# Kernel optimization log

Measured on AMD Instinct MI355X. Metric: run time of the kernel, lower is better.

Reference implementation:

```python
import jax, jax.numpy as jnp
import numpy as np

B, S, H = 8, 2048, 512
M = 4096
TEMP = 0.1
EPS = 1e-6


def setup_inputs() -> dict:
    key = jax.random.key(0)
    ks = jax.random.split(key, 8)
    scale = 1.0 / np.sqrt(H)
    return {
        "hidden_states": jax.random.normal(ks[0], (B, S, H), dtype=jnp.float32),
        "memory_keys": jax.random.normal(ks[1], (M, H), dtype=jnp.float32),
        "memory_values": jax.random.normal(ks[2], (M, H), dtype=jnp.float32),
        "Wk": jax.random.normal(ks[3], (H, H), dtype=jnp.float32) * scale,
        "bk": jnp.zeros((H,), dtype=jnp.float32),
        "Wo": jax.random.normal(ks[4], (H, H), dtype=jnp.float32) * scale,
        "bo": jnp.zeros((H,), dtype=jnp.float32),
        "memory_usage": jax.random.randint(ks[5], (M,), 0, 2, dtype=jnp.int32),
    }


def reference(hidden_states, memory_keys, memory_values, Wk, bk, Wo, bo, memory_usage):
    # key projection: [B,S,H]
    q = jnp.einsum("bsh,kh->bsk", hidden_states, Wk) + bk
    # L2-style normalization with eps inside rsqrt (matches torch.rsqrt(norm_sq + 1e-6))
    q_n = q * jax.lax.rsqrt(jnp.sum(q * q, axis=-1, keepdims=True) + EPS)
    mk_n = memory_keys * jax.lax.rsqrt(
        jnp.sum(memory_keys * memory_keys, axis=-1, keepdims=True) + EPS
    )
    # cosine-similarity scores over the memory bank: [B,S,M]
    scores = jnp.einsum("bsk,mk->bsm", q_n, mk_n) / TEMP
    mask = (memory_usage > 0).astype(scores.dtype)  # [M]
    scores = scores * mask + (-1e9) * (1.0 - mask)
    attn = jax.nn.softmax(scores, axis=-1)  # [B,S,M]
    retrieved = jnp.einsum("bsm,mv->bsv", attn, memory_values)  # [B,S,H]
    out = jnp.einsum("bsv,hv->bsh", retrieved, Wo) + bo
    return out
```

## Files before the change

### kernel.cpp

```cpp
#include <hip/hip_runtime.h>
#include <cstdint>
#include <cstddef>

#define H_DIM   512
#define M_DIM   4096

typedef unsigned short u16;
typedef short bf16x8 __attribute__((ext_vector_type(8)));
typedef float f32x4  __attribute__((ext_vector_type(4)));

__device__ __forceinline__ u16 f2b(float f) {
  union { float f; uint32_t u; } v; v.f = f;
  uint32_t u = v.u + (0x7FFFu + ((v.u >> 16) & 1u));
  return (u16)(u >> 16);
}

__global__ void k_f2bf(const float* __restrict__ in, u16* __restrict__ out, int n4) {
  int i = blockIdx.x * blockDim.x + threadIdx.x;
  if (i < n4) {
    float4 v = ((const float4*)in)[i];
    ushort4 o;
    o.x = f2b(v.x); o.y = f2b(v.y); o.z = f2b(v.z); o.w = f2b(v.w);
    ((ushort4*)out)[i] = o;
  }
}

__global__ void k_f2bf_ww(const float* __restrict__ wk, const float* __restrict__ wo,
                          u16* __restrict__ owk, u16* __restrict__ owo) {
  int i = blockIdx.x * blockDim.x + threadIdx.x;
  const float* src = (i < 65536) ? wk : wo;
  u16* dst = (i < 65536) ? owk : owo;
  int j = i & 65535;
  float4 v = ((const float4*)src)[j];
  ushort4 o;
  o.x = f2b(v.x); o.y = f2b(v.y); o.z = f2b(v.z); o.w = f2b(v.w);
  ((ushort4*)dst)[j] = o;
}

__global__ void k_compact(const int* __restrict__ usage, int* __restrict__ idx,
                          int* __restrict__ meta) {
  __shared__ int cnt[256];
  int t = threadIdx.x;
  int base = t * 16;
  int c = 0;
  #pragma unroll
  for (int i = 0; i < 16; ++i) c += (usage[base + i] > 0) ? 1 : 0;
  cnt[t] = c;
  __syncthreads();
  for (int d = 1; d < 256; d <<= 1) {
    int v = (t >= d) ? cnt[t - d] : 0;
    __syncthreads();
    cnt[t] += v;
    __syncthreads();
  }
  int pos = cnt[t] - c;
  for (int i = 0; i < 16; ++i)
    if (usage[base + i] > 0) idx[pos++] = base + i;
  if (t == 0) {
    int total = cnt[255];
    int keff = ((total + 127) >> 7) << 7;
    meta[0] = total; meta[1] = keff; meta[2] = keff >> 5; meta[3] = keff >> 7;
  }
}

__global__ void k_gather_both(const float* __restrict__ keys, const float* __restrict__ vals,
                              const int* __restrict__ idx, const int* __restrict__ meta,
                              u16* __restrict__ okeys, u16* __restrict__ ovals) {
  int j    = blockIdx.x * 4 + (threadIdx.x >> 6);
  int lane = threadIdx.x & 63;
  int count = meta[0];
  ushort4* kp = (ushort4*)(okeys + (size_t)j * H_DIM);
  ushort4* vp = (ushort4*)(ovals + (size_t)j * H_DIM);
  if (j >= count) {
    ushort4 z = {0, 0, 0, 0};
    kp[lane] = z; kp[lane + 64] = z;
    vp[lane] = z; vp[lane + 64] = z;
    return;
  }
  int src = idx[j];
  const float4* rp = (const float4*)(keys + (size_t)src * H_DIM);
  float4 a = rp[lane];
  float4 b = rp[lane + 64];
  float ss = a.x*a.x + a.y*a.y + a.z*a.z + a.w*a.w
           + b.x*b.x + b.y*b.y + b.z*b.z + b.w*b.w;
  #pragma unroll
  for (int d = 1; d < 64; d <<= 1) ss += __shfl_xor(ss, d, 64);
  float s = rsqrtf(ss + 1e-6f);
  ushort4 oa, ob;
  oa.x = f2b(a.x*s); oa.y = f2b(a.y*s); oa.z = f2b(a.z*s); oa.w = f2b(a.w*s);
  ob.x = f2b(b.x*s); ob.y = f2b(b.y*s); ob.z = f2b(b.z*s); ob.w = f2b(b.w*s);
  kp[lane]      = oa;
  kp[lane + 64] = ob;
  const float4* vr = (const float4*)(vals + (size_t)src * H_DIM);
  float4 c0 = vr[lane];
  float4 c1 = vr[lane + 64];
  ushort4 va, vb;
  va.x = f2b(c0.x); va.y = f2b(c0.y); va.z = f2b(c0.z); va.w = f2b(c0.w);
  vb.x = f2b(c1.x); vb.y = f2b(c1.y); vb.z = f2b(c1.z); vb.w = f2b(c1.w);
  vp[lane]      = va;
  vp[lane + 64] = vb;
}

__global__ void k_rsq(const float* __restrict__ qss, float* __restrict__ rsq) {
  int r = blockIdx.x * blockDim.x + threadIdx.x;
  float s = 0.0f;
  #pragma unroll
  for (int i = 0; i < 8; ++i) s += qss[(size_t)r * 8 + i];
  rsq[r] = rsqrtf(s + 1e-6f);
}

__global__ void k_reduce_l(const float* __restrict__ lpart, float* __restrict__ linv,
                           const int* __restrict__ meta) {
  int r = blockIdx.x * blockDim.x + threadIdx.x;
  int n = meta[1] >> 6;
  float s = 0.0f;
  for (int i = 0; i < n; ++i) s += lpart[(size_t)r * 64 + i];
  linv[r] = 1.0f / s;
}

#define EPI_MW    1

template<int EPI>
__global__ __launch_bounds__(256, 3)
void k_gemm_bt(const u16* __restrict__ A, const u16* __restrict__ B,
               int N, int K,
               const int* __restrict__ meta,
               u16* __restrict__ outh) {
  __shared__ u16 Ah[2][128 * 32];
  __shared__ u16 Bh[2][128 * 32];

  const int tid  = threadIdx.x;
  const int wave = tid >> 6, lane = tid & 63;
  const int wr = (wave >> 1) * 64;
  const int wc = (wave & 1) * 64;

  int t0 = blockIdx.x, t_end = meta[1] >> 7, t_step = 16;
  int fixedb = blockIdx.y;
  const int kiters = K >> 5;

  const int srow   = lane & 15;
  const int schunk = lane >> 4;
  const int lds_off = schunk * 128 + srow * 8;

  const int fr = lane & 15;
  const int fbase = (lane >> 4) * 128 + fr * 8;
  const int g = lane >> 4;

  const char* Ac = (const char*)A;
  const char* Bc = (const char*)B;

  for (int t = t0; t < t_end; t += t_step) {
    const int row0 = fixedb << 7;
    const int col0 = t << 7;
    __syncthreads();

    uint32_t aB[2], bB[2];
    #pragma unroll
    for (int s2 = 0; s2 < 2; ++s2) {
      aB[s2] = (uint32_t)(((size_t)(row0 + (wave + s2 * 4) * 16 + srow) * (size_t)K
                           + (size_t)(schunk * 8)) * 2u);
      bB[s2] = (uint32_t)(((size_t)(col0 + (wave + s2 * 4) * 16 + srow) * (size_t)K
                           + (size_t)(schunk * 8)) * 2u);
    }

    f32x4 acc[4][4];
    const f32x4 z = {0.0f, 0.0f, 0.0f, 0.0f};
    #pragma unroll
    for (int i = 0; i < 4; ++i)
      #pragma unroll
      for (int j = 0; j < 4; ++j) acc[i][j] = z;

    bf16x8 rA[2], rB[2];
    auto gload = [&](int k0) {
      const uint32_t kb = (uint32_t)(k0 << 1);
      #pragma unroll
      for (int s2 = 0; s2 < 2; ++s2) rA[s2] = *(const bf16x8*)(Ac + aB[s2] + kb);
      #pragma unroll
      for (int s2 = 0; s2 < 2; ++s2) rB[s2] = *(const bf16x8*)(Bc + bB[s2] + kb);
    };

    gload(0);
    for (int it = 0; it < kiters; ++it) {
      const int cur = it & 1;
      #pragma unroll
      for (int s2 = 0; s2 < 2; ++s2)
        *(bf16x8*)&Ah[cur][(wave + s2 * 4) * 512 + lds_off] = rA[s2];
      #pragma unroll
      for (int s2 = 0; s2 < 2; ++s2)
        *(bf16x8*)&Bh[cur][(wave + s2 * 4) * 512 + lds_off] = rB[s2];
      if (it + 1 < kiters) gload((it + 1) << 5);
      __syncthreads();

      bf16x8 af[4], bfv[4];
      #pragma unroll
      for (int i = 0; i < 4; ++i)
        af[i] = *(const bf16x8*)&Ah[cur][((wr >> 4) + i) * 512 + fbase];
      #pragma unroll
      for (int j = 0; j < 4; ++j)
        bfv[j] = *(const bf16x8*)&Bh[cur][((wc >> 4) + j) * 512 + fbase];
      #pragma unroll
      for (int i = 0; i < 4; ++i)
        #pragma unroll
        for (int j = 0; j < 4; ++j)
          acc[i][j] = __builtin_amdgcn_mfma_f32_16x16x32_bf16(af[i], bfv[j], acc[i][j], 0, 0, 0);
    }

    #pragma unroll
    for (int i = 0; i < 4; ++i) {
      #pragma unroll
      for (int r = 0; r < 4; ++r) {
        int grow = row0 + wr + i * 16 + g * 4 + r;
        #pragma unroll
        for (int j = 0; j < 4; ++j) {
          int gcol = col0 + wc + j * 16 + fr;
          outh[(size_t)grow * (size_t)N + gcol] = f2b(acc[i][j][r]);
        }
      }
    }
  }
}

#define EPI2_P     0
#define EPI2_OUT   1
#define EPI2_QPROJ 2

template<int EPI>
__global__ __launch_bounds__(512, 2)
void k_gemm2(const u16* __restrict__ A, const u16* __restrict__ B,
             const int* __restrict__ meta,
             float* __restrict__ outf, u16* __restrict__ outh,
             const float* __restrict__ bias,
             float* __restrict__ aux,
             const float* __restrict__ rowscale) {
  constexpr int BM   = (EPI == EPI2_P) ? 256 : 128;
  constexpr int MF   = BM / 32;
  constexpr int NF   = 4;
  constexpr int APS  = BM / 128;
  constexpr int NLA  = BM / 64;
  constexpr int NLB  = 4;
  constexpr int ASUB = BM * 32;
  constexpr int BSUB = 256 * 32;

  __shared__ u16 Ah[2][BM * 64];
  __shared__ u16 Bh[2][256 * 64];

  const int tid  = threadIdx.x;
  const int wave = tid >> 6, lane = tid & 63;
  const int wave_m = wave >> 2, wave_n = wave & 3;
  const int wm0 = wave_m * (BM >> 1);
  const int wn0 = wave_n * 64;
  const int fr  = lane & 15, g = lane >> 4;
  const int fbase = g * 128 + fr * 8;

  int m0, r0, kel;
  if (EPI == EPI2_P) {
    int id = blockIdx.x + (blockIdx.y << 4);
    int xcd = id & 7, s = id >> 3;
    r0 = (xcd * 8 + (s >> 4)) << 8;
    m0 = (s & 15) << 8;
    if (m0 >= meta[1]) return;
    kel = 512;
  } else if (EPI == EPI2_OUT) {
    int id = blockIdx.x + (blockIdx.y << 2);
    int xcd = id & 7, s = id >> 3;
    r0 = (xcd * 8 + (s >> 2)) << 8;
    m0 = (s & 3) << 7;
    kel = meta[1];
  } else {
    int id = blockIdx.x + (blockIdx.y << 2);
    int xcd = id & 7, s = id >> 3;
    r0 = (xcd * 8 + (s >> 2)) << 8;
    m0 = (s & 3) << 7;
    kel = 512;
  }
  const int kiters = kel >> 6;
  if (kiters <= 0) return;
  const int kstr = (EPI == EPI2_OUT) ? M_DIM : 512;

  const char* Ac = (const char*)A;
  const char* Bc = (const char*)B;
  uint32_t aB[NLA], bB[NLB];
  #pragma unroll
  for (int s2 = 0; s2 < NLA; ++s2) {
    int ks = s2 / APS;
    int u  = tid + (s2 % APS) * 512;
    int row = ((u >> 6) << 4) + (u & 15);
    int kch = (u >> 4) & 3;
    aB[s2] = (uint32_t)(((size_t)(m0 + row) * (size_t)kstr
                         + (size_t)(ks * 32 + kch * 8)) * 2u);
  }
  #pragma unroll
  for (int s2 = 0; s2 < NLB; ++s2) {
    int ks = s2 >> 1;
    int u  = tid + (s2 & 1) * 512;
    int row = ((u >> 6) << 4) + (u & 15);
    int kch = (u >> 4) & 3;
    bB[s2] = (uint32_t)(((size_t)(r0 + row) * (size_t)kstr
                         + (size_t)(ks * 32 + kch * 8)) * 2u);
  }

  f32x4 acc[MF][NF];
  const f32x4 z = {0.0f, 0.0f, 0.0f, 0.0f};
  #pragma unroll
  for (int i = 0; i < MF; ++i)
    #pragma unroll
    for (int j = 0; j < NF; ++j) acc[i][j] = z;

  auto gload = [&](bf16x8 (&ra)[NLA], bf16x8 (&rb)[NLB], int it1) {
    const uint32_t kb = (uint32_t)(it1 << 7);
    #pragma unroll
    for (int s2 = 0; s2 < NLA; ++s2) ra[s2] = *(const bf16x8*)(Ac + aB[s2] + kb);
    #pragma unroll
    for (int s2 = 0; s2 < NLB; ++s2) rb[s2] = *(const bf16x8*)(Bc + bB[s2] + kb);
  };
  auto commit = [&](int cur, bf16x8 (&ra)[NLA], bf16x8 (&rb)[NLB]) {
    #pragma unroll
    for (int s2 = 0; s2 < NLA; ++s2)
      *(bf16x8*)&Ah[cur][(s2 / APS) * ASUB + (tid + (s2 % APS) * 512) * 8] = ra[s2];
    #pragma unroll
    for (int s2 = 0; s2 < NLB; ++s2)
      *(bf16x8*)&Bh[cur][(s2 >> 1) * BSUB + (tid + (s2 & 1) * 512) * 8] = rb[s2];
  };
  auto compute = [&](int cur) {
    bf16x8 af[MF], bfv[NF];
    #pragma unroll
    for (int i = 0; i < MF; ++i)
      af[i] = *(const bf16x8*)&Ah[cur][((wm0 >> 4) + i) * 512 + fbase];
    #pragma unroll
    for (int j = 0; j < NF; ++j)
      bfv[j] = *(const bf16x8*)&Bh[cur][((wn0 >> 4) + j) * 512 + fbase];
    #pragma unroll
    for (int i = 0; i < MF; ++i)
      #pragma unroll
      for (int j = 0; j < NF; ++j)
        acc[i][j] = __builtin_amdgcn_mfma_f32_16x16x32_bf16(af[i], bfv[j], acc[i][j], 0, 0, 0);
    #pragma unroll
    for (int i = 0; i < MF; ++i)
      af[i] = *(const bf16x8*)&Ah[cur][ASUB + ((wm0 >> 4) + i) * 512 + fbase];
    #pragma unroll
    for (int j = 0; j < NF; ++j)
      bfv[j] = *(const bf16x8*)&Bh[cur][BSUB + ((wn0 >> 4) + j) * 512 + fbase];
    #pragma unroll
    for (int i = 0; i < MF; ++i)
      #pragma unroll
      for (int j = 0; j < NF; ++j)
        acc[i][j] = __builtin_amdgcn_mfma_f32_16x16x32_bf16(af[i], bfv[j], acc[i][j], 0, 0, 0);
  };

  if constexpr (EPI == EPI2_P) {
    bf16x8 rA[NLA], rB[NLB];
    gload(rA, rB, 0);
    for (int it = 0; it < kiters; ++it) {
      const int cur = it & 1;
      commit(cur, rA, rB);
      if (it + 1 < kiters) gload(rA, rB, it + 1);
      __syncthreads();
      compute(cur);
    }
  } else {
    bf16x8 a0[NLA], b0[NLB], a1[NLA], b1[NLB];
    gload(a0, b0, 0);
    if (kiters > 1) gload(a1, b1, 1);
    for (int it = 0; it < kiters; it += 2) {
      commit(0, a0, b0);
      if (it + 2 < kiters) gload(a0, b0, it + 2);
      __syncthreads();
      compute(0);
      commit(1, a1, b1);
      if (it + 3 < kiters) gload(a1, b1, it + 3);
      __syncthreads();
      compute(1);
    }
  }

  if (EPI == EPI2_P) {
    const int count = meta[0];
    float rq10[NF];
    #pragma unroll
    for (int j = 0; j < NF; ++j)
      rq10[j] = rowscale[r0 + wn0 + j * 16 + fr] * 10.0f;
    float sj[NF] = {0.f, 0.f, 0.f, 0.f};
    #pragma unroll
    for (int i = 0; i < MF; ++i) {
      const int mb = m0 + wm0 + i * 16 + g * 4;
      #pragma unroll
      for (int j = 0; j < NF; ++j) {
        const size_t rr = (size_t)(r0 + wn0 + j * 16 + fr);
        float p0 = (mb + 0 < count) ? __expf(acc[i][j][0] * rq10[j]) : 0.0f;
        float p1 = (mb + 1 < count) ? __expf(acc[i][j][1] * rq10[j]) : 0.0f;
        float p2 = (mb + 2 < count) ? __expf(acc[i][j][2] * rq10[j]) : 0.0f;
        float p3 = (mb + 3 < count) ? __expf(acc[i][j][3] * rq10[j]) : 0.0f;
        ushort4 st; st.x = f2b(p0); st.y = f2b(p1); st.z = f2b(p2); st.w = f2b(p3);
        *(ushort4*)(outh + rr * M_DIM + mb) = st;
        sj[j] += (p0 + p1) + (p2 + p3);
      }
    }
    const int slot = (m0 + wm0) >> 6;
    #pragma unroll
    for (int j = 0; j < NF; ++j) {
      float s = sj[j];
      s += __shfl_xor(s, 16, 64);
      s += __shfl_xor(s, 32, 64);
      if (lane < 16) {
        const size_t rr = (size_t)(r0 + wn0 + j * 16 + lane);
        aux[rr * 64 + slot]     = s;
        aux[rr * 64 + slot + 1] = 0.0f;
      }
    }
  } else if (EPI == EPI2_OUT) {
    float scl[NF];
    #pragma unroll
    for (int j = 0; j < NF; ++j)
      scl[j] = rowscale[r0 + wn0 + j * 16 + fr];
    #pragma unroll
    for (int i = 0; i < MF; ++i) {
      const int hb = m0 + wm0 + i * 16 + g * 4;
      const float4 bv = *(const float4*)(bias + hb);
      #pragma unroll
      for (int j = 0; j < NF; ++j) {
        const size_t rr = (size_t)(r0 + wn0 + j * 16 + fr);
        float4 o;
        o.x = acc[i][j][0] * scl[j] + bv.x;
        o.y = acc[i][j][1] * scl[j] + bv.y;
        o.z = acc[i][j][2] * scl[j] + bv.z;
        o.w = acc[i][j][3] * scl[j] + bv.w;
        *(float4*)(outf + rr * H_DIM + hb) = o;
      }
    }
  } else {
    float sj[NF] = {0.f, 0.f, 0.f, 0.f};
    #pragma unroll
    for (int i = 0; i < MF; ++i) {
      const int kb = m0 + wm0 + i * 16 + g * 4;
      const float4 bkv = *(const float4*)(bias + kb);
      #pragma unroll
      for (int j = 0; j < NF; ++j) {
        const size_t rr = (size_t)(r0 + wn0 + j * 16 + fr);
        float v0 = acc[i][j][0] + bkv.x;
        float v1 = acc[i][j][1] + bkv.y;
        float v2 = acc[i][j][2] + bkv.z;
        float v3 = acc[i][j][3] + bkv.w;
        ushort4 st; st.x = f2b(v0); st.y = f2b(v1); st.z = f2b(v2); st.w = f2b(v3);
        *(ushort4*)(outh + rr * H_DIM + kb) = st;
        sj[j] += v0 * v0 + v1 * v1 + v2 * v2 + v3 * v3;
      }
    }
    const int slot = (m0 + wm0) >> 6;
    #pragma unroll
    for (int j = 0; j < NF; ++j) {
      float s = sj[j];
      s += __shfl_xor(s, 16, 64);
      s += __shfl_xor(s, 32, 64);
      if (lane < 16)
        aux[(size_t)(r0 + wn0 + j * 16 + lane) * 8 + slot] = s;
    }
  }
}

extern "C" void kernel_launch(void* const* d_in, const int* in_sizes, int n_in,
                              void* d_out, int out_size, void* d_ws, size_t ws_size,
                              hipStream_t stream) {
  const float* hidden = (const float*)d_in[0];
  const float* mkeys  = (const float*)d_in[1];
  const float* mvals  = (const float*)d_in[2];
  const float* Wk     = (const float*)d_in[3];
  const float* bk     = (const float*)d_in[4];
  const float* Wo     = (const float*)d_in[5];
  const float* bo     = (const float*)d_in[6];
  const int*   usage  = (const int*)d_in[7];
  (void)in_sizes; (void)n_in; (void)out_size; (void)ws_size;

  char* ws = (char*)d_ws;
  u16*   hb    = (u16*)(ws + 0);
  int*   idx   = (int*)(ws + 0);
  int*   meta  = (int*)(ws + 16384);
  float* lpart = (float*)(ws + 1048576);
  u16*   wkb   = (u16*)(ws + 16777216);
  u16*   wob   = (u16*)(ws + 17301504);
  u16*   mkn   = (u16*)(ws + 17825792);
  u16*   mv_c  = (u16*)(ws + 22020096);
  u16*   qb    = (u16*)(ws + 26214400);
  u16*   MWt   = (u16*)(ws + 42991616);
  u16*   P     = (u16*)(ws + 47185920);
  float* qss   = (float*)(ws + 47185920);
  float* rsqQ  = (float*)(ws + 181665792);
  float* linv  = (float*)(ws + 183828480);

  k_f2bf<<<8192, 256, 0, stream>>>(hidden, hb, 2097152);
  k_f2bf_ww<<<512, 256, 0, stream>>>(Wk, Wo, wkb, wob);

  k_gemm2<EPI2_QPROJ><<<dim3(4, 64), 512, 0, stream>>>(wkb, hb, nullptr,
      nullptr, qb, bk, qss, nullptr);
  k_rsq<<<64, 256, 0, stream>>>(qss, rsqQ);

  k_compact<<<1, 256, 0, stream>>>(usage, idx, meta);
  k_gather_both<<<1024, 256, 0, stream>>>(mkeys, mvals, idx, meta, mkn, mv_c);

  k_gemm_bt<EPI_MW><<<dim3(16, 4), 256, 0, stream>>>(wob, mv_c, M_DIM, 512,
      meta, MWt);

  k_gemm2<EPI2_P><<<dim3(16, 64), 512, 0, stream>>>(mkn, qb, meta,
      nullptr, P, nullptr, lpart, rsqQ);
  k_reduce_l<<<64, 256, 0, stream>>>(lpart, linv, meta);

  k_gemm2<EPI2_OUT><<<dim3(4, 64), 512, 0, stream>>>(MWt, P, meta,
      (float*)d_out, nullptr, bo, nullptr, linv);
}
```

Baseline: 256.0 us.

## Restructure GEMM main loop to overlap LDS commits with MFMA and raise priority

Reorders the double-buffered GEMM pipeline so the next tile's LDS commit and global prefetch happen between the two MFMA half-steps of the current tile, with one barrier per iteration instead of commit-then-sync-then-compute. It also wraps each MFMA block in s_setprio(1)/s_setprio(0) so matrix instructions get issue priority over other waves' memory work. The intent is to hide LDS write and global load latency behind MFMA execution. In exchange, fragment registers stay live longer across the loop, which raises register pressure, and the buffer hand-off needs correct ordering to avoid races.

```diff
diff --git a/kernel.cpp b/kernel.cpp
--- a/kernel.cpp
+++ b/kernel.cpp
@@ -306,6 +306,8 @@
     #pragma unroll
     for (int j = 0; j < NF; ++j) acc[i][j] = z;
 
+  bf16x8 af[MF], bfv[NF];
+
   auto gload = [&](bf16x8 (&ra)[NLA], bf16x8 (&rb)[NLB], int it1) {
     const uint32_t kb = (uint32_t)(it1 << 7);
     #pragma unroll
@@ -321,55 +323,61 @@
     for (int s2 = 0; s2 < NLB; ++s2)
       *(bf16x8*)&Bh[cur][(s2 >> 1) * BSUB + (tid + (s2 & 1) * 512) * 8] = rb[s2];
   };
-  auto compute = [&](int cur) {
-    bf16x8 af[MF], bfv[NF];
+  auto read_frags = [&](int cur, int ks) {
     #pragma unroll
     for (int i = 0; i < MF; ++i)
-      af[i] = *(const bf16x8*)&Ah[cur][((wm0 >> 4) + i) * 512 + fbase];
+      af[i] = *(const bf16x8*)&Ah[cur][ks * ASUB + ((wm0 >> 4) + i) * 512 + fbase];
     #pragma unroll
     for (int j = 0; j < NF; ++j)
-      bfv[j] = *(const bf16x8*)&Bh[cur][((wn0 >> 4) + j) * 512 + fbase];
+      bfv[j] = *(const bf16x8*)&Bh[cur][ks * BSUB + ((wn0 >> 4) + j) * 512 + fbase];
+  };
+  auto mfma_all = [&]() {
+    __builtin_amdgcn_s_setprio(1);
     #pragma unroll
     for (int i = 0; i < MF; ++i)
       #pragma unroll
       for (int j = 0; j < NF; ++j)
         acc[i][j] = __builtin_amdgcn_mfma_f32_16x16x32_bf16(af[i], bfv[j], acc[i][j], 0, 0, 0);
-    #pragma unroll
-    for (int i = 0; i < MF; ++i)
-      af[i] = *(const bf16x8*)&Ah[cur][ASUB + ((wm0 >> 4) + i) * 512 + fbase];
-    #pragma unroll
-    for (int j = 0; j < NF; ++j)
-      bfv[j] = *(const bf16x8*)&Bh[cur][BSUB + ((wn0 >> 4) + j) * 512 + fbase];
-    #pragma unroll
-    for (int i = 0; i < MF; ++i)
-      #pragma unroll
-      for (int j = 0; j < NF; ++j)
-        acc[i][j] = __builtin_amdgcn_mfma_f32_16x16x32_bf16(af[i], bfv[j], acc[i][j], 0, 0, 0);
+    __builtin_amdgcn_s_setprio(0);
   };
 
   if constexpr (EPI == EPI2_P) {
     bf16x8 rA[NLA], rB[NLB];
     gload(rA, rB, 0);
+    commit(0, rA, rB);
+    if (kiters > 1) gload(rA, rB, 1);
+    __syncthreads();
     for (int it = 0; it < kiters; ++it) {
       const int cur = it & 1;
-      commit(cur, rA, rB);
-      if (it + 1 < kiters) gload(rA, rB, it + 1);
+      read_frags(cur, 0);
+      mfma_all();
+      read_frags(cur, 1);
+      if (it + 1 < kiters) commit(cur ^ 1, rA, rB);
+      if (it + 2 < kiters) gload(rA, rB, it + 2);
+      mfma_all();
       __syncthreads();
-      compute(cur);
     }
   } else {
     bf16x8 a0[NLA], b0[NLB], a1[NLA], b1[NLB];
     gload(a0, b0, 0);
+    commit(0, a0, b0);
     if (kiters > 1) gload(a1, b1, 1);
+    __syncthreads();
     for (int it = 0; it < kiters; it += 2) {
-      commit(0, a0, b0);
+      read_frags(0, 0);
       if (it + 2 < kiters) gload(a0, b0, it + 2);
+      mfma_all();
+      read_frags(0, 1);
+      if (it + 1 < kiters) commit(1, a1, b1);
+      mfma_all();
       __syncthreads();
-      compute(0);
-      commit(1, a1, b1);
+      read_frags(1, 0);
       if (it + 3 < kiters) gload(a1, b1, it + 3);
+      mfma_all();
+      read_frags(1, 1);
+      if (it + 2 < kiters) commit(0, a0, b0);
+      mfma_all();
       __syncthreads();
-      compute(1);
     }
   }
 
```

Result: slower. 271.4 us (+6.0%).

## Fuse fp32-to-bf16 conversions and gathers into GEMM loads, drop rsq kernel

Applied to the files above, without the earlier changes.

The q-projection GEMM now reads fp32 hidden states directly and converts to bf16 while staging into LDS, which removes the separate conversion kernel and its bf16 intermediate. The memory-values gather and conversion are folded into the MW GEMM through indexed fp32 loads. The row-norm rsqrt reduction moves into the P-GEMM epilogue, so the small k_rsq kernel goes away. The fused loaders move twice the bytes per element through registers and the MW B-operand loads are now indirect, which could cut the efficiency of the inner loops.

```diff
diff --git a/kernel.cpp b/kernel.cpp
--- a/kernel.cpp
+++ b/kernel.cpp
@@ -15,14 +15,11 @@
   return (u16)(u >> 16);
 }
 
-__global__ void k_f2bf(const float* __restrict__ in, u16* __restrict__ out, int n4) {
-  int i = blockIdx.x * blockDim.x + threadIdx.x;
-  if (i < n4) {
-    float4 v = ((const float4*)in)[i];
-    ushort4 o;
-    o.x = f2b(v.x); o.y = f2b(v.y); o.z = f2b(v.z); o.w = f2b(v.w);
-    ((ushort4*)out)[i] = o;
-  }
+__device__ __forceinline__ bf16x8 cvt8(const float4& lo, const float4& hi) {
+  union { u16 u[8]; bf16x8 v; } o;
+  o.u[0] = f2b(lo.x); o.u[1] = f2b(lo.y); o.u[2] = f2b(lo.z); o.u[3] = f2b(lo.w);
+  o.u[4] = f2b(hi.x); o.u[5] = f2b(hi.y); o.u[6] = f2b(hi.z); o.u[7] = f2b(hi.w);
+  return o.v;
 }
 
 __global__ void k_f2bf_ww(const float* __restrict__ wk, const float* __restrict__ wo,
@@ -63,18 +60,16 @@
   }
 }
 
-__global__ void k_gather_both(const float* __restrict__ keys, const float* __restrict__ vals,
+__global__ void k_gather_keys(const float* __restrict__ keys,
                               const int* __restrict__ idx, const int* __restrict__ meta,
-                              u16* __restrict__ okeys, u16* __restrict__ ovals) {
+                              u16* __restrict__ okeys) {
   int j    = blockIdx.x * 4 + (threadIdx.x >> 6);
   int lane = threadIdx.x & 63;
   int count = meta[0];
   ushort4* kp = (ushort4*)(okeys + (size_t)j * H_DIM);
-  ushort4* vp = (ushort4*)(ovals + (size_t)j * H_DIM);
   if (j >= count) {
     ushort4 z = {0, 0, 0, 0};
     kp[lane] = z; kp[lane + 64] = z;
-    vp[lane] = z; vp[lane + 64] = z;
     return;
   }
   int src = idx[j];
@@ -91,22 +86,6 @@
   ob.x = f2b(b.x*s); ob.y = f2b(b.y*s); ob.z = f2b(b.z*s); ob.w = f2b(b.w*s);
   kp[lane]      = oa;
   kp[lane + 64] = ob;
-  const float4* vr = (const float4*)(vals + (size_t)src * H_DIM);
-  float4 c0 = vr[lane];
-  float4 c1 = vr[lane + 64];
-  ushort4 va, vb;
-  va.x = f2b(c0.x); va.y = f2b(c0.y); va.z = f2b(c0.z); va.w = f2b(c0.w);
-  vb.x = f2b(c1.x); vb.y = f2b(c1.y); vb.z = f2b(c1.z); vb.w = f2b(c1.w);
-  vp[lane]      = va;
-  vp[lane + 64] = vb;
-}
-
-__global__ void k_rsq(const float* __restrict__ qss, float* __restrict__ rsq) {
-  int r = blockIdx.x * blockDim.x + threadIdx.x;
-  float s = 0.0f;
-  #pragma unroll
-  for (int i = 0; i < 8; ++i) s += qss[(size_t)r * 8 + i];
-  rsq[r] = rsqrtf(s + 1e-6f);
 }
 
 __global__ void k_reduce_l(const float* __restrict__ lpart, float* __restrict__ linv,
@@ -118,13 +97,9 @@
   linv[r] = 1.0f / s;
 }
 
-#define EPI_MW    1
-
-template<int EPI>
 __global__ __launch_bounds__(256, 3)
-void k_gemm_bt(const u16* __restrict__ A, const u16* __restrict__ B,
-               int N, int K,
-               const int* __restrict__ meta,
+void k_gemm_mw(const u16* __restrict__ A, const float* __restrict__ Bf,
+               const int* __restrict__ idx, const int* __restrict__ meta,
                u16* __restrict__ outh) {
   __shared__ u16 Ah[2][128 * 32];
   __shared__ u16 Bh[2][128 * 32];
@@ -134,9 +109,11 @@
   const int wr = (wave >> 1) * 64;
   const int wc = (wave & 1) * 64;
 
-  int t0 = blockIdx.x, t_end = meta[1] >> 7, t_step = 16;
-  int fixedb = blockIdx.y;
-  const int kiters = K >> 5;
+  const int count = meta[0];
+  if (blockIdx.x >= (meta[1] >> 7)) return;
+  const int row0 = blockIdx.y << 7;
+  const int col0 = blockIdx.x << 7;
+  const int kiters = 512 >> 5;
 
   const int srow   = lane & 15;
   const int schunk = lane >> 4;
@@ -147,74 +124,78 @@
   const int g = lane >> 4;
 
   const char* Ac = (const char*)A;
-  const char* Bc = (const char*)B;
-
-  for (int t = t0; t < t_end; t += t_step) {
-    const int row0 = fixedb << 7;
-    const int col0 = t << 7;
+
+  uint32_t aB[2];
+  uint32_t bB[2];
+  bool bval[2];
+  #pragma unroll
+  for (int s2 = 0; s2 < 2; ++s2) {
+    aB[s2] = (uint32_t)(((size_t)(row0 + (wave + s2 * 4) * 16 + srow) * 512u
+                         + (size_t)(schunk * 8)) * 2u);
+    int mrow = col0 + (wave + s2 * 4) * 16 + srow;
+    bval[s2] = (mrow < count);
+    int src = bval[s2] ? idx[mrow] : 0;
+    bB[s2] = (uint32_t)(((size_t)src * 512u + (size_t)(schunk * 8)) * 4u);
+  }
+
+  f32x4 acc[4][4];
+  const f32x4 z = {0.0f, 0.0f, 0.0f, 0.0f};
+  #pragma unroll
+  for (int i = 0; i < 4; ++i)
+    #pragma unroll
+    for (int j = 0; j < 4; ++j) acc[i][j] = z;
+
+  bf16x8 rA[2];
+  float4 rBlo[2], rBhi[2];
+  auto gload = [&](int k0) {
+    const uint32_t kb  = (uint32_t)(k0 << 1);
+    const uint32_t kbf = (uint32_t)(k0 << 2);
+    #pragma unroll
+    for (int s2 = 0; s2 < 2; ++s2) rA[s2] = *(const bf16x8*)(Ac + aB[s2] + kb);
+    #pragma unroll
+    for (int s2 = 0; s2 < 2; ++s2) {
+      rBlo[s2] = *(const float4*)((const char*)Bf + bB[s2] + kbf);
+      rBhi[s2] = *(const float4*)((const char*)Bf + bB[s2] + kbf + 16);
+    }
+  };
+
+  const float4 zf = {0.f, 0.f, 0.f, 0.f};
+  gload(0);
+  for (int it = 0; it < kiters; ++it) {
+    const int cur = it & 1;
+    #pragma unroll
+    for (int s2 = 0; s2 < 2; ++s2)
+      *(bf16x8*)&Ah[cur][(wave + s2 * 4) * 512 + lds_off] = rA[s2];
+    #pragma unroll
+    for (int s2 = 0; s2 < 2; ++s2)
+      *(bf16x8*)&Bh[cur][(wave + s2 * 4) * 512 + lds_off] =
+          bval[s2] ? cvt8(rBlo[s2], rBhi[s2]) : cvt8(zf, zf);
+    if (it + 1 < kiters) gload((it + 1) << 5);
     __syncthreads();
 
-    uint32_t aB[2], bB[2];
-    #pragma unroll
-    for (int s2 = 0; s2 < 2; ++s2) {
-      aB[s2] = (uint32_t)(((size_t)(row0 + (wave + s2 * 4) * 16 + srow) * (size_t)K
-                           + (size_t)(schunk * 8)) * 2u);
-      bB[s2] = (uint32_t)(((size_t)(col0 + (wave + s2 * 4) * 16 + srow) * (size_t)K
-                           + (size_t)(schunk * 8)) * 2u);
-    }
-
-    f32x4 acc[4][4];
-    const f32x4 z = {0.0f, 0.0f, 0.0f, 0.0f};
+    bf16x8 af[4], bfv[4];
     #pragma unroll
     for (int i = 0; i < 4; ++i)
-      #pragma unroll
-      for (int j = 0; j < 4; ++j) acc[i][j] = z;
-
-    bf16x8 rA[2], rB[2];
-    auto gload = [&](int k0) {
-      const uint32_t kb = (uint32_t)(k0 << 1);
-      #pragma unroll
-      for (int s2 = 0; s2 < 2; ++s2) rA[s2] = *(const bf16x8*)(Ac + aB[s2] + kb);
-      #pragma unroll
-      for (int s2 = 0; s2 < 2; ++s2) rB[s2] = *(const bf16x8*)(Bc + bB[s2] + kb);
-    };
-
-    gload(0);
-    for (int it = 0; it < kiters; ++it) {
-      const int cur = it & 1;
-      #pragma unroll
-      for (int s2 = 0; s2 < 2; ++s2)
-        *(bf16x8*)&Ah[cur][(wave + s2 * 4) * 512 + lds_off] = rA[s2];
-      #pragma unroll
-      for (int s2 = 0; s2 < 2; ++s2)
-        *(bf16x8*)&Bh[cur][(wave + s2 * 4) * 512 + lds_off] = rB[s2];
-      if (it + 1 < kiters) gload((it + 1) << 5);
-      __syncthreads();
-
-      bf16x8 af[4], bfv[4];
-      #pragma unroll
-      for (int i = 0; i < 4; ++i)
-        af[i] = *(const bf16x8*)&Ah[cur][((wr >> 4) + i) * 512 + fbase];
+      af[i] = *(const bf16x8*)&Ah[cur][((wr >> 4) + i) * 512 + fbase];
+    #pragma unroll
+    for (int j = 0; j < 4; ++j)
+      bfv[j] = *(const bf16x8*)&Bh[cur][((wc >> 4) + j) * 512 + fbase];
+    #pragma unroll
+    for (int i = 0; i < 4; ++i)
       #pragma unroll
       for (int j = 0; j < 4; ++j)
-        bfv[j] = *(const bf16x8*)&Bh[cur][((wc >> 4) + j) * 512 + fbase];
-      #pragma unroll
-      for (int i = 0; i < 4; ++i)
-        #pragma unroll
-        for (int j = 0; j < 4; ++j)
-          acc[i][j] = __builtin_amdgcn_mfma_f32_16x16x32_bf16(af[i], bfv[j], acc[i][j], 0, 0, 0);
-    }
-
-    #pragma unroll
-    for (int i = 0; i < 4; ++i) {
-      #pragma unroll
-      for (int r = 0; r < 4; ++r) {
-        int grow = row0 + wr + i * 16 + g * 4 + r;
-        #pragma unroll
-        for (int j = 0; j < 4; ++j) {
-          int gcol = col0 + wc + j * 16 + fr;
-          outh[(size_t)grow * (size_t)N + gcol] = f2b(acc[i][j][r]);
-        }
+        acc[i][j] = __builtin_amdgcn_mfma_f32_16x16x32_bf16(af[i], bfv[j], acc[i][j], 0, 0, 0);
+  }
+
+  #pragma unroll
+  for (int i = 0; i < 4; ++i) {
+    #pragma unroll
+    for (int r = 0; r < 4; ++r) {
+      int grow = row0 + wr + i * 16 + g * 4 + r;
+      #pragma unroll
+      for (int j = 0; j < 4; ++j) {
+        int gcol = col0 + wc + j * 16 + fr;
+        outh[(size_t)grow * (size_t)M_DIM + gcol] = f2b(acc[i][j][r]);
       }
     }
   }
@@ -240,6 +221,7 @@
   constexpr int NLB  = 4;
   constexpr int ASUB = BM * 32;
   constexpr int BSUB = 256 * 32;
+  constexpr bool BF32 = (EPI == EPI2_QPROJ);
 
   __shared__ u16 Ah[2][BM * 64];
   __shared__ u16 Bh[2][256 * 64];
@@ -296,7 +278,7 @@
     int row = ((u >> 6) << 4) + (u & 15);
     int kch = (u >> 4) & 3;
     bB[s2] = (uint32_t)(((size_t)(r0 + row) * (size_t)kstr
-                         + (size_t)(ks * 32 + kch * 8)) * 2u);
+                         + (size_t)(ks * 32 + kch * 8)) * (BF32 ? 4u : 2u));
   }
 
   f32x4 acc[MF][NF];
@@ -306,21 +288,40 @@
     #pragma unroll
     for (int j = 0; j < NF; ++j) acc[i][j] = z;
 
-  auto gload = [&](bf16x8 (&ra)[NLA], bf16x8 (&rb)[NLB], int it1) {
+  auto gloadA = [&](bf16x8 (&ra)[NLA], int it1) {
     const uint32_t kb = (uint32_t)(it1 << 7);
     #pragma unroll
     for (int s2 = 0; s2 < NLA; ++s2) ra[s2] = *(const bf16x8*)(Ac + aB[s2] + kb);
+  };
+  auto gloadBh = [&](bf16x8 (&rb)[NLB], int it1) {
+    const uint32_t kb = (uint32_t)(it1 << 7);
     #pragma unroll
     for (int s2 = 0; s2 < NLB; ++s2) rb[s2] = *(const bf16x8*)(Bc + bB[s2] + kb);
   };
-  auto commit = [&](int cur, bf16x8 (&ra)[NLA], bf16x8 (&rb)[NLB]) {
+  auto gloadBf = [&](float4 (&lo)[NLB], float4 (&hi)[NLB], int it1) {
+    const uint32_t kb = (uint32_t)(it1 << 8);
+    #pragma unroll
+    for (int s2 = 0; s2 < NLB; ++s2) {
+      lo[s2] = *(const float4*)(Bc + bB[s2] + kb);
+      hi[s2] = *(const float4*)(Bc + bB[s2] + kb + 16);
+    }
+  };
+  auto commitA = [&](int cur, bf16x8 (&ra)[NLA]) {
     #pragma unroll
     for (int s2 = 0; s2 < NLA; ++s2)
       *(bf16x8*)&Ah[cur][(s2 / APS) * ASUB + (tid + (s2 % APS) * 512) * 8] = ra[s2];
+  };
+  auto commitBh = [&](int cur, bf16x8 (&rb)[NLB]) {
     #pragma unroll
     for (int s2 = 0; s2 < NLB; ++s2)
       *(bf16x8*)&Bh[cur][(s2 >> 1) * BSUB + (tid + (s2 & 1) * 512) * 8] = rb[s2];
   };
+  auto commitBf = [&](int cur, float4 (&lo)[NLB], float4 (&hi)[NLB]) {
+    #pragma unroll
+    for (int s2 = 0; s2 < NLB; ++s2)
+      *(bf16x8*)&Bh[cur][(s2 >> 1) * BSUB + (tid + (s2 & 1) * 512) * 8] =
+          cvt8(lo[s2], hi[s2]);
+  };
   auto compute = [&](int cur) {
     bf16x8 af[MF], bfv[NF];
     #pragma unroll
@@ -349,25 +350,40 @@
 
   if constexpr (EPI == EPI2_P) {
     bf16x8 rA[NLA], rB[NLB];
-    gload(rA, rB, 0);
+    gloadA(rA, 0); gloadBh(rB, 0);
     for (int it = 0; it < kiters; ++it) {
       const int cur = it & 1;
-      commit(cur, rA, rB);
-      if (it + 1 < kiters) gload(rA, rB, it + 1);
+      commitA(cur, rA); commitBh(cur, rB);
+      if (it + 1 < kiters) { gloadA(rA, it + 1); gloadBh(rB, it + 1); }
       __syncthreads();
       compute(cur);
     }
-  } else {
+  } else if constexpr (!BF32) {
     bf16x8 a0[NLA], b0[NLB], a1[NLA], b1[NLB];
-    gload(a0, b0, 0);
-    if (kiters > 1) gload(a1, b1, 1);
+    gloadA(a0, 0); gloadBh(b0, 0);
+    if (kiters > 1) { gloadA(a1, 1); gloadBh(b1, 1); }
     for (int it = 0; it < kiters; it += 2) {
-      commit(0, a0, b0);
-      if (it + 2 < kiters) gload(a0, b0, it + 2);
+      commitA(0, a0); commitBh(0, b0);
+      if (it + 2 < kiters) { gloadA(a0, it + 2); gloadBh(b0, it + 2); }
       __syncthreads();
       compute(0);
-      commit(1, a1, b1);
-      if (it + 3 < kiters) gload(a1, b1, it + 3);
+      commitA(1, a1); commitBh(1, b1);
+      if (it + 3 < kiters) { gloadA(a1, it + 3); gloadBh(b1, it + 3); }
+      __syncthreads();
+      compute(1);
+    }
+  } else {
+    bf16x8 a0[NLA], a1[NLA];
+    float4 b0lo[NLB], b0hi[NLB], b1lo[NLB], b1hi[NLB];
+    gloadA(a0, 0); gloadBf(b0lo, b0hi, 0);
+    if (kiters > 1) { gloadA(a1, 1); gloadBf(b1lo, b1hi, 1); }
+    for (int it = 0; it < kiters; it += 2) {
+      commitA(0, a0); commitBf(0, b0lo, b0hi);
+      if (it + 2 < kiters) { gloadA(a0, it + 2); gloadBf(b0lo, b0hi, it + 2); }
+      __syncthreads();
+      compute(0);
+      commitA(1, a1); commitBf(1, b1lo, b1hi);
+      if (it + 3 < kiters) { gloadA(a1, it + 3); gloadBf(b1lo, b1hi, it + 3); }
       __syncthreads();
       compute(1);
     }
@@ -377,8 +393,13 @@
     const int count = meta[0];
     float rq10[NF];
     #pragma unroll
-    for (int j = 0; j < NF; ++j)
-      rq10[j] = rowscale[r0 + wn0 + j * 16 + fr] * 10.0f;
+    for (int j = 0; j < NF; ++j) {
+      const size_t rr = (size_t)(r0 + wn0 + j * 16 + fr);
+      float ssum = 0.0f;
+      #pragma unroll
+      for (int i = 0; i < 8; ++i) ssum += rowscale[rr * 8 + i];
+      rq10[j] = rsqrtf(ssum + 1e-6f) * 10.0f;
+    }
     float sj[NF] = {0.f, 0.f, 0.f, 0.f};
     #pragma unroll
     for (int i = 0; i < MF; ++i) {
@@ -471,36 +492,30 @@
   (void)in_sizes; (void)n_in; (void)out_size; (void)ws_size;
 
   char* ws = (char*)d_ws;
-  u16*   hb    = (u16*)(ws + 0);
   int*   idx   = (int*)(ws + 0);
   int*   meta  = (int*)(ws + 16384);
   float* lpart = (float*)(ws + 1048576);
+  float* qss   = (float*)(ws + 5242880);
   u16*   wkb   = (u16*)(ws + 16777216);
   u16*   wob   = (u16*)(ws + 17301504);
   u16*   mkn   = (u16*)(ws + 17825792);
-  u16*   mv_c  = (u16*)(ws + 22020096);
   u16*   qb    = (u16*)(ws + 26214400);
   u16*   MWt   = (u16*)(ws + 42991616);
   u16*   P     = (u16*)(ws + 47185920);
-  float* qss   = (float*)(ws + 47185920);
-  float* rsqQ  = (float*)(ws + 181665792);
   float* linv  = (float*)(ws + 183828480);
 
-  k_f2bf<<<8192, 256, 0, stream>>>(hidden, hb, 2097152);
   k_f2bf_ww<<<512, 256, 0, stream>>>(Wk, Wo, wkb, wob);
 
-  k_gemm2<EPI2_QPROJ><<<dim3(4, 64), 512, 0, stream>>>(wkb, hb, nullptr,
-      nullptr, qb, bk, qss, nullptr);
-  k_rsq<<<64, 256, 0, stream>>>(qss, rsqQ);
-
   k_compact<<<1, 256, 0, stream>>>(usage, idx, meta);
-  k_gather_both<<<1024, 256, 0, stream>>>(mkeys, mvals, idx, meta, mkn, mv_c);
-
-  k_gemm_bt<EPI_MW><<<dim3(16, 4), 256, 0, stream>>>(wob, mv_c, M_DIM, 512,
-      meta, MWt);
+  k_gather_keys<<<1024, 256, 0, stream>>>(mkeys, idx, meta, mkn);
+
+  k_gemm2<EPI2_QPROJ><<<dim3(4, 64), 512, 0, stream>>>(wkb, (const u16*)hidden,
+      nullptr, nullptr, qb, bk, qss, nullptr);
+
+  k_gemm_mw<<<dim3(16, 4), 256, 0, stream>>>(wob, mvals, idx, meta, MWt);
 
   k_gemm2<EPI2_P><<<dim3(16, 64), 512, 0, stream>>>(mkn, qb, meta,
-      nullptr, P, nullptr, lpart, rsqQ);
+      nullptr, P, nullptr, lpart, qss);
   k_reduce_l<<<64, 256, 0, stream>>>(lpart, linv, meta);
 
   k_gemm2<EPI2_OUT><<<dim3(4, 64), 512, 0, stream>>>(MWt, P, meta,
```

Measured after the change: 252.5 us. No clear change (-1.4%).
